# Kernel tuning notes

Hardware: AMD Instinct MI355X
Metric: run time of the kernel (lower is better)

## Reference

```python
import jax, jax.numpy as jnp
import numpy as np

NUM_HEADS = 8


def _forward(x, Wq, bq, Wk, bk, Wv, bv, Wo, bo, w1, b1, w2, b2, tau):
    B, S, E = x.shape
    H = NUM_HEADS
    hd = E // H
    scale = hd ** -0.5

    def heads(t):
        return t.reshape(B, S, H, hd).transpose(0, 2, 1, 3)  # [B,H,S,hd]

    q = heads(x @ Wq + bq)
    k = heads(x @ Wk + bk)
    v = heads(x @ Wv + bv)
    s = jnp.einsum('bhqd,bhkd->bhqk', q, k) * scale  # [B,H,S,S]

    # ---- autopoietic transform (vectorized over batch, no mask) ----
    s = jnp.clip(jnp.nan_to_num(s, nan=0.0, posinf=10.0, neginf=-10.0), -15.0, 15.0)
    ma = s.mean(axis=1)  # mean over heads -> [B,S,S]
    eps_safe = 0.05  # clamp(eps=1e-6, 0.05, 0.8)
    sa = jnp.clip(jnp.clip(ma, -8.0, 8.0) * eps_safe, -10.0, 10.0)
    # 1x1 conv on [1,1,S,S] == per-channel scalar scale+bias -> [B,C,S,S]
    hid = jax.nn.relu(jnp.clip(sa[:, None] * w1[None, :, None, None]
                               + b1[None, :, None, None], -5.0, 5.0))
    ap = jnp.clip(jnp.einsum('bcij,c->bij', hid, w2) + b2, -5.0, 5.0)
    taylor = jnp.clip(1.0 + 0.05 * (ap * 50.0), 0.5, 1.5)
    sig = jax.nn.sigmoid(taylor)
    p = jax.nn.softmax(jnp.clip(ma, -10.0, 10.0), axis=-1)
    Hent = -p * jnp.log(p + 1e-6)
    Fm = jax.nn.softmax(3.0 * Hent, axis=-1)
    t = sig * Fm
    eo = jnp.sqrt((ma * ma).sum(axis=(1, 2), keepdims=True)) + 1e-4  # fro norm
    et = jnp.sqrt((t * t).sum(axis=(1, 2), keepdims=True)) + 1e-4
    t = jnp.clip(eo / et, 0.8, 1.2) * t
    tm = t.mean(axis=(1, 2), keepdims=True)
    om = ma.mean(axis=(1, 2), keepdims=True)
    tstd = jnp.sqrt(jnp.clip(((t - tm) ** 2).mean(axis=(1, 2), keepdims=True), 0.01, None))
    ostd = jnp.sqrt(jnp.clip(((ma - om) ** 2).mean(axis=(1, 2), keepdims=True), 0.01, None))
    gd = jnp.clip(ostd / tstd, 0.8, 1.2)
    ar = jnp.clip(jnp.abs(ma).max(axis=(1, 2), keepdims=True), 1.0, 10.0)
    sm = jnp.clip(0.3 / jnp.log1p(ar), 0.1, 0.5)
    st = tm + sm * gd * (t - tm)  # scaled_transform
    ent = Hent.mean(axis=(1, 2), keepdims=True)
    ne = ent / jnp.log(jnp.float32(S))  # normalized entropy (max_entropy = log S)
    rr = 0.4 * (1.0 - jnp.clip(ne, 0.0, 0.4))  # residual ratio (base 0.4, entropy-damped)
    # blend transform back into per-head scores (res_scale = 1.0)
    s = s + rr[:, None] * (st - ma)[:, None]

    attn = jax.nn.softmax(s / tau, axis=-1)
    out = jnp.einsum('bhqk,bhkd->bhqd', attn, v)
    out = out.transpose(0, 2, 1, 3).reshape(B, S, E)
    return out @ Wo + bo


def setup_inputs() -> dict:
    key = jax.random.key(0)
    ks = jax.random.split(key, 8)
    B, S, E, C = 4, 512, 512, 128
    w_scale = 0.02
    return {
        'x': jax.random.normal(ks[0], (B, S, E), dtype=jnp.float32),
        'Wq': jax.random.normal(ks[1], (E, E), dtype=jnp.float32) * w_scale,
        'bq': jnp.zeros((E,), jnp.float32),
        'Wk': jax.random.normal(ks[2], (E, E), dtype=jnp.float32) * w_scale,
        'bk': jnp.zeros((E,), jnp.float32),
        'Wv': jax.random.normal(ks[3], (E, E), dtype=jnp.float32) * w_scale,
        'bv': jnp.zeros((E,), jnp.float32),
        'Wo': jax.random.normal(ks[4], (E, E), dtype=jnp.float32) * w_scale,
        'bo': jnp.zeros((E,), jnp.float32),
        'w1': jax.random.normal(ks[5], (C,), dtype=jnp.float32) * 0.5,
        'b1': jnp.zeros((C,), jnp.float32),
        'w2': jax.random.normal(ks[6], (C,), dtype=jnp.float32) * 0.1,
        'b2': jnp.zeros((1,), jnp.float32),
        'tau': jnp.ones((1,), jnp.float32),
    }


def reference(x, Wq, bq, Wk, bk, Wv, bv, Wo, bo, w1, b1, w2, b2, tau):
    return _forward(x, Wq, bq, Wk, bk, Wv, bv, Wo, bo, w1, b1, w2, b2, tau)
```

## Files before the change

kernel.cpp:

```cpp
#include <hip/hip_runtime.h>
#include <math.h>

#define BB 4
#define SS 512
#define EE 512
#define NH 8
#define HD 64
#define NC 128
#define NTAB 4096

typedef _Float16 f16x8 __attribute__((ext_vector_type(8)));
typedef float f32x4 __attribute__((ext_vector_type(4)));

struct HL { _Float16 h, l; };

__device__ __forceinline__ float clampf(float v, float lo, float hi) {
  return fminf(fmaxf(v, lo), hi);
}
__device__ __forceinline__ HL split16(float x) {
  HL r;
  r.h = (_Float16)x;
  r.l = (_Float16)(x - (float)r.h);
  return r;
}

__device__ __forceinline__ float waveRedSum(float v) {
#pragma unroll
  for (int o = 32; o; o >>= 1) v += __shfl_xor(v, o);
  return v;
}
__device__ __forceinline__ float waveRedMax(float v) {
#pragma unroll
  for (int o = 32; o; o >>= 1) v = fmaxf(v, __shfl_xor(v, o));
  return v;
}
__device__ __forceinline__ float blockRedSum(float v, float* red) {
  int tid = threadIdx.x;
  v = waveRedSum(v);
  __syncthreads();
  if ((tid & 63) == 0) red[tid >> 6] = v;
  __syncthreads();
  return red[0] + red[1] + red[2] + red[3];
}
__device__ __forceinline__ float blockRedMax(float v, float* red) {
  int tid = threadIdx.x;
  v = waveRedMax(v);
  __syncthreads();
  if ((tid & 63) == 0) red[tid >> 6] = v;
  __syncthreads();
  return fmaxf(fmaxf(red[0], red[1]), fmaxf(red[2], red[3]));
}

__global__ __launch_bounds__(256) void k_prep(
    const float* __restrict__ w1, const float* __restrict__ b1,
    const float* __restrict__ w2, const float* __restrict__ b2,
    float* __restrict__ T, const float* __restrict__ x,
    _Float16* __restrict__ xh, _Float16* __restrict__ xl,
    const float* __restrict__ Wq, const float* __restrict__ Wk,
    const float* __restrict__ Wv, const float* __restrict__ Wo,
    _Float16* __restrict__ Wth, _Float16* __restrict__ Wtl) {
  const int bid = blockIdx.x;
  const int tid = threadIdx.x;
  if (bid < 17) {
    int idx = bid * 256 + tid;
    if (idx > NTAB) return;
    float sa = -0.4f + (float)idx * (0.8f / (float)NTAB);
    float ap = 0.f;
#pragma unroll 4
    for (int c = 0; c < NC; ++c) {
      float h = fminf(fmaxf(sa * w1[c] + b1[c], 0.f), 5.f);
      ap += h * w2[c];
    }
    ap = clampf(ap + b2[0], -5.f, 5.f);
    float tay = clampf(1.0f + 0.05f * (ap * 50.0f), 0.5f, 1.5f);
    T[idx] = 1.0f / (1.0f + expf(-tay));
  } else if (bid < 529) {
    int idx = ((bid - 17) * 256 + tid) * 8;
    float4 u0 = *(const float4*)(x + idx);
    float4 u1 = *(const float4*)(x + idx + 4);
    float f[8] = {u0.x, u0.y, u0.z, u0.w, u1.x, u1.y, u1.z, u1.w};
    f16x8 h, l;
#pragma unroll
    for (int j = 0; j < 8; ++j) {
      HL r = split16(f[j]);
      h[j] = r.h;
      l[j] = r.l;
    }
    *(f16x8*)(xh + idx) = h;
    *(f16x8*)(xl + idx) = l;
  } else {
    const int j = bid - 529;
    const int z = j >> 6;
    const int rem = j & 63;
    const int k0 = (rem & 7) * 64, n0 = (rem >> 3) * 64;
    const float* W = (z == 0) ? Wq : (z == 1) ? Wk : (z == 2) ? Wv : Wo;
    __shared__ float Tt[64][68];
    const int r = tid >> 2, c = (tid & 3) * 16;
#pragma unroll
    for (int jj = 0; jj < 16; jj += 4)
      *(float4*)&Tt[r][c + jj] =
          *(const float4*)(W + (size_t)(k0 + r) * EE + n0 + c + jj);
    __syncthreads();
    f16x8 h0, l0, h1, l1;
#pragma unroll
    for (int jj = 0; jj < 8; ++jj) {
      HL r0 = split16(Tt[c + jj][r]);
      HL r1 = split16(Tt[c + 8 + jj][r]);
      h0[jj] = r0.h; l0[jj] = r0.l;
      h1[jj] = r1.h; l1[jj] = r1.l;
    }
    _Float16* dh = Wth + ((size_t)z * EE + n0 + r) * EE + k0 + c;
    _Float16* dl = Wtl + ((size_t)z * EE + n0 + r) * EE + k0 + c;
    *(f16x8*)dh = h0;
    *(f16x8*)(dh + 8) = h1;
    *(f16x8*)dl = l0;
    *(f16x8*)(dl + 8) = l1;
  }
}

__global__ __launch_bounds__(256) void k_qkv_mfma(
    const _Float16* __restrict__ xh, const _Float16* __restrict__ xl,
    const _Float16* __restrict__ Wth, const _Float16* __restrict__ Wtl,
    const float* __restrict__ bq, const float* __restrict__ bk,
    const float* __restrict__ bv,
    _Float16* __restrict__ qh, _Float16* __restrict__ ql,
    _Float16* __restrict__ kh, _Float16* __restrict__ kl,
    _Float16* __restrict__ vth, _Float16* __restrict__ vtl) {
  const int which = blockIdx.z;
  const int tid = threadIdx.x;
  const int wave = tid >> 6, lane = tid & 63;
  const int quad = lane >> 4, l16 = lane & 15;
  const int m0 = blockIdx.y * 64;
  const int n0 = blockIdx.x * 64;
  const _Float16* Bh = Wth + (size_t)which * EE * EE;
  const _Float16* Bl = Wtl + (size_t)which * EE * EE;

  __shared__ __align__(16) char smpool[36864];
  _Float16(*LAh)[72] = (_Float16(*)[72])(smpool);
  _Float16(*LAl)[72] = (_Float16(*)[72])(smpool + 9216);
  _Float16(*LBh)[72] = (_Float16(*)[72])(smpool + 18432);
  _Float16(*LBl)[72] = (_Float16(*)[72])(smpool + 27648);
  float(*TR)[68] = (float(*)[68])(smpool);

  const int sr0 = tid >> 3, sc0 = (tid & 7) * 8;
  const int sr1 = (tid + 256) >> 3, sc1 = sc0;

  f32x4 acc[4] = {};
  for (int k0 = 0; k0 < EE; k0 += 64) {
    if (k0) __syncthreads();
    *(f16x8*)&LAh[sr0][sc0] = *(const f16x8*)(xh + (size_t)(m0 + sr0) * EE + k0 + sc0);
    *(f16x8*)&LAl[sr0][sc0] = *(const f16x8*)(xl + (size_t)(m0 + sr0) * EE + k0 + sc0);
    *(f16x8*)&LBh[sr0][sc0] = *(const f16x8*)(Bh + (size_t)(n0 + sr0) * EE + k0 + sc0);
    *(f16x8*)&LBl[sr0][sc0] = *(const f16x8*)(Bl + (size_t)(n0 + sr0) * EE + k0 + sc0);
    *(f16x8*)&LAh[sr1][sc1] = *(const f16x8*)(xh + (size_t)(m0 + sr1) * EE + k0 + sc1);
    *(f16x8*)&LAl[sr1][sc1] = *(const f16x8*)(xl + (size_t)(m0 + sr1) * EE + k0 + sc1);
    *(f16x8*)&LBh[sr1][sc1] = *(const f16x8*)(Bh + (size_t)(n0 + sr1) * EE + k0 + sc1);
    *(f16x8*)&LBl[sr1][sc1] = *(const f16x8*)(Bl + (size_t)(n0 + sr1) * EE + k0 + sc1);
    __syncthreads();
#pragma unroll
    for (int kk = 0; kk < 64; kk += 32) {
      f16x8 ah = *(const f16x8*)&LAh[wave * 16 + l16][kk + quad * 8];
      f16x8 al = *(const f16x8*)&LAl[wave * 16 + l16][kk + quad * 8];
#pragma unroll
      for (int nt = 0; nt < 4; ++nt) {
        f16x8 bhf = *(const f16x8*)&LBh[nt * 16 + l16][kk + quad * 8];
        f16x8 blf = *(const f16x8*)&LBl[nt * 16 + l16][kk + quad * 8];
        acc[nt] = __builtin_amdgcn_mfma_f32_16x16x32_f16(ah, bhf, acc[nt], 0, 0, 0);
        acc[nt] = __builtin_amdgcn_mfma_f32_16x16x32_f16(ah, blf, acc[nt], 0, 0, 0);
        acc[nt] = __builtin_amdgcn_mfma_f32_16x16x32_f16(al, bhf, acc[nt], 0, 0, 0);
      }
    }
  }
  const float* bias = (which == 0) ? bq : (which == 1) ? bk : bv;
  if (which == 2) {
    __syncthreads();
#pragma unroll
    for (int nt = 0; nt < 4; ++nt) {
      const int dcol = nt * 16 + l16;
      const float bb = bias[n0 + nt * 16 + l16];
#pragma unroll
      for (int r = 0; r < 4; ++r)
        TR[dcol][wave * 16 + quad * 4 + r] = acc[nt][r] + bb;
    }
    __syncthreads();
    const int d = tid >> 2, cc = (tid & 3) * 16;
    const int bh = (m0 >> 9) * NH + (n0 >> 6);
    const int si0 = m0 & 511;
    f16x8 h0, l0, h1, l1;
#pragma unroll
    for (int jj = 0; jj < 8; ++jj) {
      HL r0 = split16(TR[d][cc + jj]);
      HL r1 = split16(TR[d][cc + 8 + jj]);
      h0[jj] = r0.h; l0[jj] = r0.l;
      h1[jj] = r1.h; l1[jj] = r1.l;
    }
    _Float16* dh = vth + ((size_t)bh * HD + d) * SS + si0 + cc;
    _Float16* dl = vtl + ((size_t)bh * HD + d) * SS + si0 + cc;
    *(f16x8*)dh = h0;
    *(f16x8*)(dh + 8) = h1;
    *(f16x8*)dl = l0;
    *(f16x8*)(dl + 8) = l1;
  } else {
    const float postscale = (which == 0) ? 0.125f : 1.0f;
    const int mbase = m0 + wave * 16 + quad * 4;
#pragma unroll
    for (int nt = 0; nt < 4; ++nt) {
      const int col = n0 + nt * 16 + l16;
      const float bb = bias[col];
      const int hh = col >> 6, d = col & 63;
#pragma unroll
      for (int r = 0; r < 4; ++r) {
        const int mm = mbase + r;
        const int b_ = mm >> 9, si = mm & 511;
        const size_t idx = (((size_t)(b_ * NH + hh)) * SS + si) * HD + d;
        const float val = (acc[nt][r] + bb) * postscale;
        HL sp = split16(val);
        (which ? kh : qh)[idx] = sp.h;
        (which ? kl : ql)[idx] = sp.l;
      }
    }
  }
}

__global__ __launch_bounds__(256) void k_scores_mfma(
    const _Float16* __restrict__ qh, const _Float16* __restrict__ ql,
    const _Float16* __restrict__ kh, const _Float16* __restrict__ kl,
    float* __restrict__ s) {
  const int bh = blockIdx.z;
  const int i0 = blockIdx.y * 64, j0 = blockIdx.x * 64;
  const int tid = threadIdx.x;
  const int wave = tid >> 6, lane = tid & 63;
  const int quad = lane >> 4, l16 = lane & 15;

  const size_t qoff = ((size_t)bh * SS + i0 + wave * 16 + l16) * HD + quad * 8;
  f16x8 a_hi[2], a_lo[2];
#pragma unroll
  for (int ks = 0; ks < 2; ++ks) {
    a_hi[ks] = *(const f16x8*)(qh + qoff + ks * 32);
    a_lo[ks] = *(const f16x8*)(ql + qoff + ks * 32);
  }
  f16x8 b_hi[4][2], b_lo[4][2];
#pragma unroll
  for (int t = 0; t < 4; ++t) {
    const size_t koff = ((size_t)bh * SS + j0 + t * 16 + l16) * HD + quad * 8;
#pragma unroll
    for (int ks = 0; ks < 2; ++ks) {
      b_hi[t][ks] = *(const f16x8*)(kh + koff + ks * 32);
      b_lo[t][ks] = *(const f16x8*)(kl + koff + ks * 32);
    }
  }
  f32x4 acc[4] = {};
#pragma unroll
  for (int ks = 0; ks < 2; ++ks) {
#pragma unroll
    for (int t = 0; t < 4; ++t) {
      acc[t] = __builtin_amdgcn_mfma_f32_16x16x32_f16(a_hi[ks], b_hi[t][ks],
                                                      acc[t], 0, 0, 0);
      acc[t] = __builtin_amdgcn_mfma_f32_16x16x32_f16(a_hi[ks], b_lo[t][ks],
                                                      acc[t], 0, 0, 0);
      acc[t] = __builtin_amdgcn_mfma_f32_16x16x32_f16(a_lo[ks], b_hi[t][ks],
                                                      acc[t], 0, 0, 0);
    }
  }
  float* sb = s + (size_t)bh * SS * SS;
#pragma unroll
  for (int t = 0; t < 4; ++t) {
#pragma unroll
    for (int r = 0; r < 4; ++r) {
      float val = clampf(acc[t][r], -15.0f, 15.0f);
      sb[(size_t)(i0 + wave * 16 + quad * 4 + r) * SS + j0 + t * 16 + l16] = val;
    }
  }
}

__global__ __launch_bounds__(64) void k_rowstat(
    const float* __restrict__ s, const float* __restrict__ T,
    float* __restrict__ ma, float* __restrict__ t_un,
    float* __restrict__ rowred) {
  const int row = blockIdx.x;
  const int b_ = row >> 9, i = row & 511;
  const int lane = threadIdx.x;

  float4 a0 = {0.f, 0.f, 0.f, 0.f}, a1 = {0.f, 0.f, 0.f, 0.f};
#pragma unroll
  for (int hh = 0; hh < NH; ++hh) {
    const float4* p = reinterpret_cast<const float4*>(
                          s + (((size_t)(b_ * NH + hh) * SS) + i) * SS) +
                      lane * 2;
    float4 u0 = p[0], u1 = p[1];
    a0.x += u0.x; a0.y += u0.y; a0.z += u0.z; a0.w += u0.w;
    a1.x += u1.x; a1.y += u1.y; a1.z += u1.z; a1.w += u1.w;
  }
  float m[8] = {a0.x * 0.125f, a0.y * 0.125f, a0.z * 0.125f, a0.w * 0.125f,
                a1.x * 0.125f, a1.y * 0.125f, a1.z * 0.125f, a1.w * 0.125f};
  {
    float4* mp = reinterpret_cast<float4*>(ma + ((size_t)b_ * SS + i) * SS) +
                 lane * 2;
    float4 w0 = {m[0], m[1], m[2], m[3]}, w1v = {m[4], m[5], m[6], m[7]};
    mp[0] = w0;
    mp[1] = w1v;
  }
  float sma = 0.f, sma2 = 0.f, mabs = 0.f;
#pragma unroll
  for (int e = 0; e < 8; ++e) {
    sma += m[e];
    sma2 += m[e] * m[e];
    mabs = fmaxf(mabs, fabsf(m[e]));
  }
  sma = waveRedSum(sma);
  sma2 = waveRedSum(sma2);
  mabs = waveRedMax(mabs);

  float ex[8], esum = 0.f;
#pragma unroll
  for (int e = 0; e < 8; ++e) {
    ex[e] = expf(clampf(m[e], -10.f, 10.f));
    esum += ex[e];
  }
  esum = waveRedSum(esum);
  float inv = 1.0f / esum;
  float Hv[8], sH = 0.f;
#pragma unroll
  for (int e = 0; e < 8; ++e) {
    float p = ex[e] * inv;
    Hv[e] = -p * logf(p + 1e-6f);
    sH += Hv[e];
  }
  sH = waveRedSum(sH);

  float fx[8], fsum = 0.f;
#pragma unroll
  for (int e = 0; e < 8; ++e) {
    fx[e] = expf(3.0f * Hv[e]);
    fsum += fx[e];
  }
  fsum = waveRedSum(fsum);
  float finv = 1.0f / fsum;

  float t[8], st = 0.f, st2 = 0.f;
#pragma unroll
  for (int e = 0; e < 8; ++e) {
    float sa = clampf(m[e], -8.f, 8.f) * 0.05f;
    float pos = (sa + 0.4f) * ((float)NTAB / 0.8f);
    int idx = (int)pos;
    idx = idx < 0 ? 0 : (idx > NTAB - 1 ? NTAB - 1 : idx);
    float frac = pos - (float)idx;
    float g0 = T[idx], g1 = T[idx + 1];
    float sig = g0 + (g1 - g0) * frac;
    t[e] = sig * fx[e] * finv;
    st += t[e];
    st2 += t[e] * t[e];
  }
  st = waveRedSum(st);
  st2 = waveRedSum(st2);
  {
    float4* tp = reinterpret_cast<float4*>(t_un + ((size_t)b_ * SS + i) * SS) +
                 lane * 2;
    float4 w0 = {t[0], t[1], t[2], t[3]}, w1v = {t[4], t[5], t[6], t[7]};
    tp[0] = w0;
    tp[1] = w1v;
  }
  if (lane == 0) {
    float* rp = rowred + (size_t)row * 8;
    rp[0] = sma; rp[1] = sma2; rp[2] = mabs;
    rp[3] = st;  rp[4] = st2;  rp[5] = sH;
  }
}

__global__ __launch_bounds__(256) void k_consts(
    const float* __restrict__ rowred, float* __restrict__ cst) {
  const int b_ = blockIdx.x;
  const int tid = threadIdx.x;
  __shared__ float red[4];
  const float* r0 = rowred + ((size_t)b_ * SS + tid * 2) * 8;
  const float* r1 = r0 + 8;
  float sma = blockRedSum(r0[0] + r1[0], red);
  float sma2 = blockRedSum(r0[1] + r1[1], red);
  float mabs = blockRedMax(fmaxf(r0[2], r1[2]), red);
  float st = blockRedSum(r0[3] + r1[3], red);
  float st2 = blockRedSum(r0[4] + r1[4], red);
  float sH = blockRedSum(r0[5] + r1[5], red);
  if (tid == 0) {
    const float N = (float)(SS * SS);
    float eo = sqrtf(sma2) + 1e-4f;
    float et = sqrtf(st2) + 1e-4f;
    float r = clampf(eo / et, 0.8f, 1.2f);
    float tmean = r * st / N;
    float om = sma / N;
    float vart = r * r * fmaxf(st2 / N - (st / N) * (st / N), 0.f);
    float tstd = sqrtf(fmaxf(vart, 0.01f));
    float varo = fmaxf(sma2 / N - om * om, 0.f);
    float ostd = sqrtf(fmaxf(varo, 0.01f));
    float gd = clampf(ostd / tstd, 0.8f, 1.2f);
    float ar = clampf(mabs, 1.f, 10.f);
    float sm = clampf(0.3f / log1pf(ar), 0.1f, 0.5f);
    float ent = sH / N;
    float ne = ent / logf((float)SS);
    float rr = 0.4f * (1.f - clampf(ne, 0.f, 0.4f));
    float G = sm * gd;
    cst[b_ * 4 + 0] = rr * (1.f - G) * tmean;
    cst[b_ * 4 + 1] = rr * G * r;
    cst[b_ * 4 + 2] = rr;
  }
}

__global__ __launch_bounds__(64) void k_blend(
    const float* __restrict__ s, const float* __restrict__ ma,
    const float* __restrict__ t_un, const float* __restrict__ cst,
    const float* __restrict__ tau, _Float16* __restrict__ ph,
    _Float16* __restrict__ pl) {
  const int rid = blockIdx.x;
  const int bh = rid >> 9, i = rid & 511;
  const int b_ = bh >> 3;
  const int lane = threadIdx.x;
  const float c0 = cst[b_ * 4 + 0], c1 = cst[b_ * 4 + 1], c2 = cst[b_ * 4 + 2];
  const float itau = 1.0f / tau[0];
  const size_t rowbase = ((size_t)bh * SS + i) * SS;
  const float* srow = s + rowbase;
  const float* mrow = ma + ((size_t)b_ * SS + i) * SS;
  const float* trow = t_un + ((size_t)b_ * SS + i) * SS;

  float e[8], sum = 0.f;
#pragma unroll
  for (int u = 0; u < 2; ++u) {
    float4 sv = ((const float4*)srow)[lane * 2 + u];
    float4 mv = ((const float4*)mrow)[lane * 2 + u];
    float4 tv = ((const float4*)trow)[lane * 2 + u];
    const float* sp = (const float*)&sv;
    const float* mp = (const float*)&mv;
    const float* tp = (const float*)&tv;
#pragma unroll
    for (int j = 0; j < 4; ++j) {
      float vv = (sp[j] + c0 + c1 * tp[j] - c2 * mp[j]) * itau;
      e[u * 4 + j] = expf(vv);
      sum += e[u * 4 + j];
    }
  }
  sum = waveRedSum(sum);
  const float inv = 1.0f / sum;
  f16x8 hv, lv;
#pragma unroll
  for (int j = 0; j < 8; ++j) {
    HL r = split16(e[j] * inv);
    hv[j] = r.h;
    lv[j] = r.l;
  }
  *(f16x8*)(ph + rowbase + lane * 8) = hv;
  *(f16x8*)(pl + rowbase + lane * 8) = lv;
}

__global__ __launch_bounds__(256) void k_av_mfma(
    const _Float16* __restrict__ ph, const _Float16* __restrict__ pl,
    const _Float16* __restrict__ vth, const _Float16* __restrict__ vtl,
    _Float16* __restrict__ oh, _Float16* __restrict__ ol) {
  const int bh = blockIdx.z;
  const int b_ = bh >> 3, hh = bh & 7;
  const int nh = blockIdx.x;
  const int tid = threadIdx.x;
  const int wave = tid >> 6, lane = tid & 63;
  const int quad = lane >> 4, l16 = lane & 15;
  const int m0 = blockIdx.x == blockIdx.x ? blockIdx.y * 64 + wave * 16 : 0;

  f32x4 acc[2] = {};
  for (int k0 = 0; k0 < SS; k0 += 32) {
    const size_t aoff = ((size_t)bh * SS + m0 + l16) * SS + k0 + quad * 8;
    f16x8 ah = *(const f16x8*)(ph + aoff);
    f16x8 al = *(const f16x8*)(pl + aoff);
#pragma unroll
    for (int nt = 0; nt < 2; ++nt) {
      const size_t boff =
          ((size_t)bh * HD + nh * 32 + nt * 16 + l16) * SS + k0 + quad * 8;
      f16x8 bh_ = *(const f16x8*)(vth + boff);
      f16x8 bl_ = *(const f16x8*)(vtl + boff);
      acc[nt] = __builtin_amdgcn_mfma_f32_16x16x32_f16(ah, bh_, acc[nt], 0, 0, 0);
      acc[nt] = __builtin_amdgcn_mfma_f32_16x16x32_f16(ah, bl_, acc[nt], 0, 0, 0);
      acc[nt] = __builtin_amdgcn_mfma_f32_16x16x32_f16(al, bh_, acc[nt], 0, 0, 0);
    }
  }
#pragma unroll
  for (int nt = 0; nt < 2; ++nt) {
#pragma unroll
    for (int r = 0; r < 4; ++r) {
      const int si = m0 + quad * 4 + r;
      const size_t idx = ((size_t)(b_ * SS + si)) * EE + hh * HD + nh * 32 +
                         nt * 16 + l16;
      HL sp = split16(acc[nt][r]);
      oh[idx] = sp.h;
      ol[idx] = sp.l;
    }
  }
}

__global__ __launch_bounds__(256) void k_out_mfma(
    const _Float16* __restrict__ oh, const _Float16* __restrict__ ol,
    const _Float16* __restrict__ Wth, const _Float16* __restrict__ Wtl,
    const float* __restrict__ bo, float* __restrict__ out) {
  const int tid = threadIdx.x;
  const int wave = tid >> 6, lane = tid & 63;
  const int quad = lane >> 4, l16 = lane & 15;
  const int m0 = blockIdx.y * 64;
  const int n0 = blockIdx.x * 64;
  const _Float16* Bh = Wth + (size_t)3 * EE * EE;
  const _Float16* Bl = Wtl + (size_t)3 * EE * EE;

  __shared__ _Float16 LAh[64][72], LAl[64][72], LBh[64][72], LBl[64][72];

  const int sr0 = tid >> 3, sc0 = (tid & 7) * 8;
  const int sr1 = (tid + 256) >> 3, sc1 = sc0;

  f32x4 acc[4] = {};
  for (int k0 = 0; k0 < EE; k0 += 64) {
    if (k0) __syncthreads();
    *(f16x8*)&LAh[sr0][sc0] = *(const f16x8*)(oh + (size_t)(m0 + sr0) * EE + k0 + sc0);
    *(f16x8*)&LAl[sr0][sc0] = *(const f16x8*)(ol + (size_t)(m0 + sr0) * EE + k0 + sc0);
    *(f16x8*)&LBh[sr0][sc0] = *(const f16x8*)(Bh + (size_t)(n0 + sr0) * EE + k0 + sc0);
    *(f16x8*)&LBl[sr0][sc0] = *(const f16x8*)(Bl + (size_t)(n0 + sr0) * EE + k0 + sc0);
    *(f16x8*)&LAh[sr1][sc1] = *(const f16x8*)(oh + (size_t)(m0 + sr1) * EE + k0 + sc1);
    *(f16x8*)&LAl[sr1][sc1] = *(const f16x8*)(ol + (size_t)(m0 + sr1) * EE + k0 + sc1);
    *(f16x8*)&LBh[sr1][sc1] = *(const f16x8*)(Bh + (size_t)(n0 + sr1) * EE + k0 + sc1);
    *(f16x8*)&LBl[sr1][sc1] = *(const f16x8*)(Bl + (size_t)(n0 + sr1) * EE + k0 + sc1);
    __syncthreads();
#pragma unroll
    for (int kk = 0; kk < 64; kk += 32) {
      f16x8 ah = *(const f16x8*)&LAh[wave * 16 + l16][kk + quad * 8];
      f16x8 al = *(const f16x8*)&LAl[wave * 16 + l16][kk + quad * 8];
#pragma unroll
      for (int nt = 0; nt < 4; ++nt) {
        f16x8 bhf = *(const f16x8*)&LBh[nt * 16 + l16][kk + quad * 8];
        f16x8 blf = *(const f16x8*)&LBl[nt * 16 + l16][kk + quad * 8];
        acc[nt] = __builtin_amdgcn_mfma_f32_16x16x32_f16(ah, bhf, acc[nt], 0, 0, 0);
        acc[nt] = __builtin_amdgcn_mfma_f32_16x16x32_f16(ah, blf, acc[nt], 0, 0, 0);
        acc[nt] = __builtin_amdgcn_mfma_f32_16x16x32_f16(al, bhf, acc[nt], 0, 0, 0);
      }
    }
  }
  const int mbase = m0 + wave * 16 + quad * 4;
#pragma unroll
  for (int nt = 0; nt < 4; ++nt) {
    const int col = n0 + nt * 16 + l16;
    const float bb = bo[col];
#pragma unroll
    for (int r = 0; r < 4; ++r) {
      const int m = mbase + r;
      out[(size_t)m * EE + col] = acc[nt][r] + bb;
    }
  }
}

extern "C" void kernel_launch(void* const* d_in, const int* in_sizes, int n_in,
                              void* d_out, int out_size, void* d_ws,
                              size_t ws_size, hipStream_t stream) {
  const float* x = (const float*)d_in[0];
  const float* Wq = (const float*)d_in[1];
  const float* bq = (const float*)d_in[2];
  const float* Wk = (const float*)d_in[3];
  const float* bk = (const float*)d_in[4];
  const float* Wv = (const float*)d_in[5];
  const float* bv = (const float*)d_in[6];
  const float* Wo = (const float*)d_in[7];
  const float* bo = (const float*)d_in[8];
  const float* w1 = (const float*)d_in[9];
  const float* b1 = (const float*)d_in[10];
  const float* w2 = (const float*)d_in[11];
  const float* b2 = (const float*)d_in[12];
  const float* tau = (const float*)d_in[13];
  float* out = (float*)d_out;

  const size_t NX = (size_t)2048 * EE;
  const size_t NW = (size_t)4 * EE * EE;
  const size_t NQK = (size_t)BB * NH * SS * HD;
  const size_t NS = (size_t)BB * NH * SS * SS;

  _Float16* xh = (_Float16*)d_ws;
  _Float16* xl = xh + NX;
  _Float16* Wth = xl + NX;
  _Float16* Wtl = Wth + NW;
  _Float16* qh = Wtl + NW;
  _Float16* ql = qh + NQK;
  _Float16* kh = ql + NQK;
  _Float16* kl = kh + NQK;
  _Float16* vth = kl + NQK;
  _Float16* vtl = vth + NQK;
  float* s = (float*)(vtl + NQK);
  float* ma = s + NS;
  float* t_un = ma + (size_t)BB * SS * SS;
  float* T = t_un + (size_t)BB * SS * SS;
  float* rowred = T + 8192;
  float* cst = rowred + 2048 * 8;
  _Float16* ph = (_Float16*)(cst + 16);
  _Float16* pl = ph + NS;
  _Float16* oh = xh;
  _Float16* ol = xl;

  k_prep<<<785, 256, 0, stream>>>(w1, b1, w2, b2, T, x, xh, xl, Wq, Wk, Wv, Wo,
                                  Wth, Wtl);
  k_qkv_mfma<<<dim3(8, 32, 3), 256, 0, stream>>>(xh, xl, Wth, Wtl, bq, bk, bv,
                                                 qh, ql, kh, kl, vth, vtl);
  k_scores_mfma<<<dim3(8, 8, 32), 256, 0, stream>>>(qh, ql, kh, kl, s);
  k_rowstat<<<2048, 64, 0, stream>>>(s, T, ma, t_un, rowred);
  k_consts<<<4, 256, 0, stream>>>(rowred, cst);
  k_blend<<<16384, 64, 0, stream>>>(s, ma, t_un, cst, tau, ph, pl);
  k_av_mfma<<<dim3(2, 8, 32), 256, 0, stream>>>(ph, pl, vth, vtl, oh, ol);
  k_out_mfma<<<dim3(8, 32), 256, 0, stream>>>(oh, ol, Wth, Wtl, bo, out);
}
```

Before: 191.4 us.

## Stage Q/K and P tiles in LDS for scores and AV MFMA kernels

The scores kernel now loads the 64x64 Q and K hi/lo tiles cooperatively into padded shared memory, and each wave reads its MFMA fragments from there. Before, every wave fetched all K fragments straight from global memory. The AV kernel is re-tiled so each block covers 64 rows by all 64 head dims, with each wave owning 16 output columns. P chunks are staged through LDS with register prefetch of the next chunk, so each P tile is read from global once per block instead of once per column half. The cost is extra barriers, LDS traffic, and a smaller AV grid (256 blocks instead of 512).

```diff
diff --git a/kernel.cpp b/kernel.cpp
--- a/kernel.cpp
+++ b/kernel.cpp
@@ -232,43 +232,50 @@
   const int wave = tid >> 6, lane = tid & 63;
   const int quad = lane >> 4, l16 = lane & 15;
 
-  const size_t qoff = ((size_t)bh * SS + i0 + wave * 16 + l16) * HD + quad * 8;
+  __shared__ _Float16 Qh[64][72], Ql[64][72], Kh[64][72], Kl[64][72];
+  const int r = tid >> 2, c = (tid & 3) * 16;
+  {
+    const size_t qoff = ((size_t)bh * SS + i0 + r) * HD + c;
+    const size_t koff = ((size_t)bh * SS + j0 + r) * HD + c;
+    *(f16x8*)&Qh[r][c] = *(const f16x8*)(qh + qoff);
+    *(f16x8*)&Qh[r][c + 8] = *(const f16x8*)(qh + qoff + 8);
+    *(f16x8*)&Ql[r][c] = *(const f16x8*)(ql + qoff);
+    *(f16x8*)&Ql[r][c + 8] = *(const f16x8*)(ql + qoff + 8);
+    *(f16x8*)&Kh[r][c] = *(const f16x8*)(kh + koff);
+    *(f16x8*)&Kh[r][c + 8] = *(const f16x8*)(kh + koff + 8);
+    *(f16x8*)&Kl[r][c] = *(const f16x8*)(kl + koff);
+    *(f16x8*)&Kl[r][c + 8] = *(const f16x8*)(kl + koff + 8);
+  }
+  __syncthreads();
+
   f16x8 a_hi[2], a_lo[2];
 #pragma unroll
   for (int ks = 0; ks < 2; ++ks) {
-    a_hi[ks] = *(const f16x8*)(qh + qoff + ks * 32);
-    a_lo[ks] = *(const f16x8*)(ql + qoff + ks * 32);
-  }
-  f16x8 b_hi[4][2], b_lo[4][2];
+    a_hi[ks] = *(const f16x8*)&Qh[wave * 16 + l16][ks * 32 + quad * 8];
+    a_lo[ks] = *(const f16x8*)&Ql[wave * 16 + l16][ks * 32 + quad * 8];
+  }
+  f32x4 acc[4] = {};
+#pragma unroll
+  for (int ks = 0; ks < 2; ++ks) {
+#pragma unroll
+    for (int t = 0; t < 4; ++t) {
+      f16x8 b_hi = *(const f16x8*)&Kh[t * 16 + l16][ks * 32 + quad * 8];
+      f16x8 b_lo = *(const f16x8*)&Kl[t * 16 + l16][ks * 32 + quad * 8];
+      acc[t] = __builtin_amdgcn_mfma_f32_16x16x32_f16(a_hi[ks], b_hi,
+                                                      acc[t], 0, 0, 0);
+      acc[t] = __builtin_amdgcn_mfma_f32_16x16x32_f16(a_hi[ks], b_lo,
+                                                      acc[t], 0, 0, 0);
+      acc[t] = __builtin_amdgcn_mfma_f32_16x16x32_f16(a_lo[ks], b_hi,
+                                                      acc[t], 0, 0, 0);
+    }
+  }
+  float* sb = s + (size_t)bh * SS * SS;
 #pragma unroll
   for (int t = 0; t < 4; ++t) {
-    const size_t koff = ((size_t)bh * SS + j0 + t * 16 + l16) * HD + quad * 8;
-#pragma unroll
-    for (int ks = 0; ks < 2; ++ks) {
-      b_hi[t][ks] = *(const f16x8*)(kh + koff + ks * 32);
-      b_lo[t][ks] = *(const f16x8*)(kl + koff + ks * 32);
-    }
-  }
-  f32x4 acc[4] = {};
-#pragma unroll
-  for (int ks = 0; ks < 2; ++ks) {
-#pragma unroll
-    for (int t = 0; t < 4; ++t) {
-      acc[t] = __builtin_amdgcn_mfma_f32_16x16x32_f16(a_hi[ks], b_hi[t][ks],
-                                                      acc[t], 0, 0, 0);
-      acc[t] = __builtin_amdgcn_mfma_f32_16x16x32_f16(a_hi[ks], b_lo[t][ks],
-                                                      acc[t], 0, 0, 0);
-      acc[t] = __builtin_amdgcn_mfma_f32_16x16x32_f16(a_lo[ks], b_hi[t][ks],
-                                                      acc[t], 0, 0, 0);
-    }
-  }
-  float* sb = s + (size_t)bh * SS * SS;
-#pragma unroll
-  for (int t = 0; t < 4; ++t) {
-#pragma unroll
-    for (int r = 0; r < 4; ++r) {
-      float val = clampf(acc[t][r], -15.0f, 15.0f);
-      sb[(size_t)(i0 + wave * 16 + quad * 4 + r) * SS + j0 + t * 16 + l16] = val;
+#pragma unroll
+    for (int r2 = 0; r2 < 4; ++r2) {
+      float val = clampf(acc[t][r2], -15.0f, 15.0f);
+      sb[(size_t)(i0 + wave * 16 + quad * 4 + r2) * SS + j0 + t * 16 + l16] = val;
     }
   }
 }
@@ -453,38 +460,50 @@
     const _Float16* __restrict__ ph, const _Float16* __restrict__ pl,
     const _Float16* __restrict__ vth, const _Float16* __restrict__ vtl,
     _Float16* __restrict__ oh, _Float16* __restrict__ ol) {
-  const int bh = blockIdx.z;
+  const int bh = blockIdx.y;
   const int b_ = bh >> 3, hh = bh & 7;
-  const int nh = blockIdx.x;
+  const int m0 = blockIdx.x * 64;
   const int tid = threadIdx.x;
   const int wave = tid >> 6, lane = tid & 63;
   const int quad = lane >> 4, l16 = lane & 15;
-  const int m0 = blockIdx.x == blockIdx.x ? blockIdx.y * 64 + wave * 16 : 0;
-
-  f32x4 acc[2] = {};
+
+  __shared__ _Float16 Ph[64][40], Pl[64][40];
+  const int srow = tid >> 2, schunk = (tid & 3) * 8;
+  const size_t pbase = ((size_t)bh * SS + m0 + srow) * SS + schunk;
+
+  f16x8 rh = *(const f16x8*)(ph + pbase);
+  f16x8 rl = *(const f16x8*)(pl + pbase);
+
+  f32x4 acc[4] = {};
   for (int k0 = 0; k0 < SS; k0 += 32) {
-    const size_t aoff = ((size_t)bh * SS + m0 + l16) * SS + k0 + quad * 8;
-    f16x8 ah = *(const f16x8*)(ph + aoff);
-    f16x8 al = *(const f16x8*)(pl + aoff);
-#pragma unroll
-    for (int nt = 0; nt < 2; ++nt) {
-      const size_t boff =
-          ((size_t)bh * HD + nh * 32 + nt * 16 + l16) * SS + k0 + quad * 8;
-      f16x8 bh_ = *(const f16x8*)(vth + boff);
-      f16x8 bl_ = *(const f16x8*)(vtl + boff);
-      acc[nt] = __builtin_amdgcn_mfma_f32_16x16x32_f16(ah, bh_, acc[nt], 0, 0, 0);
-      acc[nt] = __builtin_amdgcn_mfma_f32_16x16x32_f16(ah, bl_, acc[nt], 0, 0, 0);
-      acc[nt] = __builtin_amdgcn_mfma_f32_16x16x32_f16(al, bh_, acc[nt], 0, 0, 0);
-    }
-  }
-#pragma unroll
-  for (int nt = 0; nt < 2; ++nt) {
+    if (k0) __syncthreads();
+    *(f16x8*)&Ph[srow][schunk] = rh;
+    *(f16x8*)&Pl[srow][schunk] = rl;
+    __syncthreads();
+    if (k0 + 32 < SS) {
+      rh = *(const f16x8*)(ph + pbase + k0 + 32);
+      rl = *(const f16x8*)(pl + pbase + k0 + 32);
+    }
+    const size_t boff = ((size_t)bh * HD + wave * 16 + l16) * SS + k0 + quad * 8;
+    f16x8 bh_ = *(const f16x8*)(vth + boff);
+    f16x8 bl_ = *(const f16x8*)(vtl + boff);
+#pragma unroll
+    for (int mt = 0; mt < 4; ++mt) {
+      f16x8 ah = *(const f16x8*)&Ph[mt * 16 + l16][quad * 8];
+      f16x8 al = *(const f16x8*)&Pl[mt * 16 + l16][quad * 8];
+      acc[mt] = __builtin_amdgcn_mfma_f32_16x16x32_f16(ah, bh_, acc[mt], 0, 0, 0);
+      acc[mt] = __builtin_amdgcn_mfma_f32_16x16x32_f16(ah, bl_, acc[mt], 0, 0, 0);
+      acc[mt] = __builtin_amdgcn_mfma_f32_16x16x32_f16(al, bh_, acc[mt], 0, 0, 0);
+    }
+  }
+#pragma unroll
+  for (int mt = 0; mt < 4; ++mt) {
 #pragma unroll
     for (int r = 0; r < 4; ++r) {
-      const int si = m0 + quad * 4 + r;
-      const size_t idx = ((size_t)(b_ * SS + si)) * EE + hh * HD + nh * 32 +
-                         nt * 16 + l16;
-      HL sp = split16(acc[nt][r]);
+      const int si = m0 + mt * 16 + quad * 4 + r;
+      const size_t idx =
+          ((size_t)(b_ * SS + si)) * EE + hh * HD + wave * 16 + l16;
+      HL sp = split16(acc[mt][r]);
       oh[idx] = sp.h;
       ol[idx] = sp.l;
     }
@@ -600,6 +619,6 @@
   k_rowstat<<<2048, 64, 0, stream>>>(s, T, ma, t_un, rowred);
   k_consts<<<4, 256, 0, stream>>>(rowred, cst);
   k_blend<<<16384, 64, 0, stream>>>(s, ma, t_un, cst, tau, ph, pl);
-  k_av_mfma<<<dim3(2, 8, 32), 256, 0, stream>>>(ph, pl, vth, vtl, oh, ol);
+  k_av_mfma<<<dim3(8, 32), 256, 0, stream>>>(ph, pl, vth, vtl, oh, ol);
   k_out_mfma<<<dim3(8, 32), 256, 0, stream>>>(oh, ol, Wth, Wtl, bo, out);
 }
```

Result: faster. 171.3 us (-10.5%).
